# Optimization experiments

Measured on AMD Instinct MI355X. Metric: run time of the kernel, lower is better.

## Reference

```python
import jax, jax.numpy as jnp
import numpy as np

FS = 44100
RESAMPLING_FACTOR = 32
N_SINES = 256
TWO_PI = 2.0 * np.pi


def linear_upsample(x, scale):
    """Match torch F.interpolate(mode='linear', align_corners=False) with integer scale_factor.
    x: [B, C, N] -> [B, C, N*scale]
    """
    n = x.shape[-1]
    out_n = n * scale
    # source coordinate for each output index (area-pixel convention)
    src = (jnp.arange(out_n, dtype=jnp.float32) + 0.5) / scale - 0.5
    src = jnp.clip(src, 0.0, n - 1)
    i0 = jnp.floor(src).astype(jnp.int32)
    i1 = jnp.minimum(i0 + 1, n - 1)
    w = (src - i0.astype(jnp.float32)).astype(x.dtype)
    return x[..., i0] * (1.0 - w) + x[..., i1] * w


def setup_inputs() -> dict:
    key = jax.random.key(0)
    k1, k2 = jax.random.split(key)
    B, S, N = 4, N_SINES, 512
    # realistic audible frequencies and normalized amplitudes
    frequencies = jax.random.uniform(k1, (B, S, N), dtype=jnp.float32) * 5000.0 + 40.0
    amplitudes = jax.random.uniform(k2, (B, S, N), dtype=jnp.float32) / S
    return {"frequencies": frequencies, "amplitudes": amplitudes}


def reference(frequencies, amplitudes):
    # upsample control signals: [B, S, N] -> [B, S, N*R]
    freqs_up = linear_upsample(frequencies, RESAMPLING_FACTOR)
    amps_up = linear_upsample(amplitudes, RESAMPLING_FACTOR)
    omegas = freqs_up * (TWO_PI / FS)
    phases = jnp.cumsum(omegas, axis=-1)
    phases = phases % TWO_PI
    # weighted sum over sines, keepdim -> [B, 1, N*R]
    signal = jnp.sum(amps_up * jnp.sin(phases), axis=1, keepdims=True)
    return signal
```

## Files before the change

### kernel.cpp

```cpp
#include <hip/hip_runtime.h>
#include <hip/hip_bf16.h>

constexpr int S = 256;
constexpr int N = 512;
constexpr int R = 32;
constexpr int OUT_N = N * R;

__global__ __launch_bounds__(512) void block_prefix_kernel(
    const float* __restrict__ freq, double* __restrict__ G) {
  const int row = blockIdx.x;
  const int n = threadIdx.x;
  const float* f = freq + (size_t)row * N;

  __shared__ double sh[N];
  float fn  = f[n];
  float fnp = (n < N - 1) ? f[n + 1] : 0.0f;
  sh[n] = (n < N - 1) ? 16.0 * ((double)fn + (double)fnp) : 0.0;
  __syncthreads();

  for (int off = 1; off < N; off <<= 1) {
    double add = (n >= off) ? sh[n - off] : 0.0;
    __syncthreads();
    sh[n] += add;
    __syncthreads();
  }

  double g = 16.0 * (double)f[0] + ((n == 0) ? 0.0 : sh[n - 1]);
  G[(size_t)row * N + n] = g;
}

__global__ __launch_bounds__(256) void synth_kernel(
    const float* __restrict__ freq, const float* __restrict__ amp,
    const double* __restrict__ G, float* __restrict__ out) {
  const int tid = threadIdx.x;
  const int split = tid >> 6;
  const int samp = tid & 63;
  const int gid = blockIdx.x * 64 + samp;
  const int b = gid >> 14;
  const int j = gid & (OUT_N - 1);

  int n;
  double c1, c2, gsel;
  float wa;
  if (j < 16) {
    n = 0; c1 = (double)(j + 1); c2 = 0.0; gsel = 0.0; wa = 0.0f;
  } else if (j >= OUT_N - 16) {
    n = N - 1; c1 = (double)(j - (OUT_N - 16) + 1); c2 = 0.0; gsel = 1.0; wa = 0.0f;
  } else {
    const int jj = j - 16;
    n = jj >> 5;
    const int k = jj & 31;
    c1 = (double)(k + 1);
    c2 = (double)((k + 1) * (k + 1)) * (1.0 / 64.0);
    gsel = 1.0;
    wa = ((float)k + 0.5f) * (1.0f / 32.0f);
  }
  const int dn1 = min(n + 1, N - 1) - n;

  const float* frow = freq + ((size_t)b * S) * N + n;
  const float* arow = amp  + ((size_t)b * S) * N + n;
  const double* grow = G   + ((size_t)b * S) * N + n;

  const double inv_fs = 1.0 / 44100.0;
  float acc = 0.0f;
  const int s0 = split * (S / 4);
  #pragma unroll 4
  for (int s = s0; s < s0 + S / 4; ++s) {
    const float* fp = frow + (size_t)s * N;
    const float* ap = arow + (size_t)s * N;
    const float fn  = fp[0];
    const float fn1 = fp[dn1];
    const float an  = ap[0];
    const float an1 = ap[dn1];
    const double g = grow[(size_t)s * N];

    double ph = fma(gsel, g, fma(c1, (double)fn,
                                 c2 * ((double)fn1 - (double)fn)));
    double r = ph * inv_fs;
    r -= floor(r);
    const float sv = __builtin_amdgcn_sinf((float)r);
    const float av = fmaf(an1 - an, wa, an);
    acc = fmaf(av, sv, acc);
  }

  __shared__ float red[256];
  red[tid] = acc;
  __syncthreads();
  if (tid < 64) {
    const float v = red[tid] + red[tid + 64] + red[tid + 128] + red[tid + 192];
    out[gid] = v;
  }
}

extern "C" void kernel_launch(void* const* d_in, const int* in_sizes, int n_in,
                              void* d_out, int out_size, void* d_ws, size_t ws_size,
                              hipStream_t stream) {
  const float* freq = (const float*)d_in[0];
  const float* amp  = (const float*)d_in[1];
  float* out = (float*)d_out;
  double* G = (double*)d_ws;

  const int B = in_sizes[0] / (S * N);

  block_prefix_kernel<<<dim3(B * S), dim3(512), 0, stream>>>(freq, G);
  synth_kernel<<<dim3(B * OUT_N / 64), dim3(256), 0, stream>>>(freq, amp, G, out);
}
```

Baseline: 78.17 us.

## Pack per-segment phase and amplitude data, reduce phase mod in prep, use fp32 synth

The prefix kernel now uses one wavefront per row with a serial per-thread scan plus shuffle scan. It reduces the cumulative phase modulo the sample rate in double, then writes an interleaved 8-float record (phase, f, df, a, da) per control point. The synth kernel then reads one packed record per sine and evaluates the phase polynomial in fp32 instead of fp64. It also uses 512-thread blocks splitting sines across 8 waves. This removes fp64 arithmetic and scattered loads from the hot loop, at the cost of some fp32 phase precision and a larger workspace.

```diff
diff --git a/kernel.cpp b/kernel.cpp
--- a/kernel.cpp
+++ b/kernel.cpp
@@ -1,37 +1,67 @@
 #include <hip/hip_runtime.h>
-#include <hip/hip_bf16.h>
 
 constexpr int S = 256;
 constexpr int N = 512;
 constexpr int R = 32;
 constexpr int OUT_N = N * R;
 
-__global__ __launch_bounds__(512) void block_prefix_kernel(
-    const float* __restrict__ freq, double* __restrict__ G) {
+__global__ __launch_bounds__(64) void prep_pack_kernel(
+    const float* __restrict__ freq, const float* __restrict__ amp,
+    float* __restrict__ W) {
   const int row = blockIdx.x;
-  const int n = threadIdx.x;
-  const float* f = freq + (size_t)row * N;
+  const int l = threadIdx.x;
+  const float* f = freq + (size_t)row * N + l * 8;
+  const float* a = amp  + (size_t)row * N + l * 8;
 
-  __shared__ double sh[N];
-  float fn  = f[n];
-  float fnp = (n < N - 1) ? f[n + 1] : 0.0f;
-  sh[n] = (n < N - 1) ? 16.0 * ((double)fn + (double)fnp) : 0.0;
-  __syncthreads();
+  const float4 fa = *reinterpret_cast<const float4*>(f);
+  const float4 fb = *reinterpret_cast<const float4*>(f + 4);
+  const float4 aa = *reinterpret_cast<const float4*>(a);
+  const float4 ab = *reinterpret_cast<const float4*>(a + 4);
 
-  for (int off = 1; off < N; off <<= 1) {
-    double add = (n >= off) ? sh[n - off] : 0.0;
-    __syncthreads();
-    sh[n] += add;
-    __syncthreads();
+  float fv[9] = {fa.x, fa.y, fa.z, fa.w, fb.x, fb.y, fb.z, fb.w, 0.0f};
+  float av[9] = {aa.x, aa.y, aa.z, aa.w, ab.x, ab.y, ab.z, ab.w, 0.0f};
+  fv[8] = __shfl_down(fa.x, 1);
+  av[8] = __shfl_down(aa.x, 1);
+
+  double p[8];
+  double run = 0.0;
+  #pragma unroll
+  for (int i = 0; i < 8; ++i) {
+    const int n = l * 8 + i;
+    const double inc =
+        (n < N - 1) ? 16.0 * ((double)fv[i] + (double)fv[i + 1]) : 0.0;
+    run += inc;
+    p[i] = run;
   }
 
-  double g = 16.0 * (double)f[0] + ((n == 0) ? 0.0 : sh[n - 1]);
-  G[(size_t)row * N + n] = g;
+  double x = run;
+  #pragma unroll
+  for (int off = 1; off < 64; off <<= 1) {
+    const double y = __shfl_up(x, off);
+    if (l >= off) x += y;
+  }
+  const double excl = x - run;
+  const float f0 = __shfl(fa.x, 0);
+  const double base = 16.0 * (double)f0;
+
+  float* wrow = W + ((size_t)row * N + l * 8) * 8;
+  #pragma unroll
+  for (int i = 0; i < 8; ++i) {
+    const int n = l * 8 + i;
+    const double g = base + excl + (i ? p[i - 1] : 0.0);
+    const double gm = g - floor(g / 44100.0) * 44100.0;
+    const float fn = fv[i];
+    const float df = (n < N - 1) ? fv[i + 1] - fn : 0.0f;
+    const float an = av[i];
+    const float da = (n < N - 1) ? av[i + 1] - an : 0.0f;
+    const float4 o{(float)gm, fn, df, an};
+    *reinterpret_cast<float4*>(wrow + i * 8) = o;
+    wrow[i * 8 + 4] = da;
+  }
 }
 
-__global__ __launch_bounds__(256) void synth_kernel(
-    const float* __restrict__ freq, const float* __restrict__ amp,
-    const double* __restrict__ G, float* __restrict__ out) {
+__global__ __launch_bounds__(512) void synth_sin_kernel(
+    const float* __restrict__ W, float* __restrict__ out) {
   const int tid = threadIdx.x;
   const int split = tid >> 6;
   const int samp = tid & 63;
@@ -40,54 +70,43 @@
   const int j = gid & (OUT_N - 1);
 
   int n;
-  double c1, c2, gsel;
-  float wa;
+  float c1, c2, wa;
   if (j < 16) {
-    n = 0; c1 = (double)(j + 1); c2 = 0.0; gsel = 0.0; wa = 0.0f;
+    n = 0; c1 = (float)(j - 15); c2 = 0.0f; wa = 0.0f;
   } else if (j >= OUT_N - 16) {
-    n = N - 1; c1 = (double)(j - (OUT_N - 16) + 1); c2 = 0.0; gsel = 1.0; wa = 0.0f;
+    n = N - 1; c1 = (float)(j - (OUT_N - 16) + 1); c2 = 0.0f; wa = 0.0f;
   } else {
     const int jj = j - 16;
     n = jj >> 5;
     const int k = jj & 31;
-    c1 = (double)(k + 1);
-    c2 = (double)((k + 1) * (k + 1)) * (1.0 / 64.0);
-    gsel = 1.0;
+    c1 = (float)(k + 1);
+    c2 = (float)((k + 1) * (k + 1)) * (1.0f / 64.0f);
     wa = ((float)k + 0.5f) * (1.0f / 32.0f);
   }
-  const int dn1 = min(n + 1, N - 1) - n;
 
-  const float* frow = freq + ((size_t)b * S) * N + n;
-  const float* arow = amp  + ((size_t)b * S) * N + n;
-  const double* grow = G   + ((size_t)b * S) * N + n;
-
-  const double inv_fs = 1.0 / 44100.0;
+  const float* wp = W + (((size_t)b * S + split * (S / 8)) * N + n) * 8;
+  constexpr float inv_fs = 1.0f / 44100.0f;
   float acc = 0.0f;
-  const int s0 = split * (S / 4);
-  #pragma unroll 4
-  for (int s = s0; s < s0 + S / 4; ++s) {
-    const float* fp = frow + (size_t)s * N;
-    const float* ap = arow + (size_t)s * N;
-    const float fn  = fp[0];
-    const float fn1 = fp[dn1];
-    const float an  = ap[0];
-    const float an1 = ap[dn1];
-    const double g = grow[(size_t)s * N];
-
-    double ph = fma(gsel, g, fma(c1, (double)fn,
-                                 c2 * ((double)fn1 - (double)fn)));
-    double r = ph * inv_fs;
-    r -= floor(r);
-    const float sv = __builtin_amdgcn_sinf((float)r);
-    const float av = fmaf(an1 - an, wa, an);
+  #pragma unroll 8
+  for (int s = 0; s < S / 8; ++s) {
+    const float4 v = *reinterpret_cast<const float4*>(wp);
+    const float da = wp[4];
+    float P = fmaf(c2, v.z, fmaf(c1, v.y, v.x));
+    float r = P * inv_fs;
+    r = r - floorf(r);
+    const float sv = __builtin_amdgcn_sinf(r);
+    const float av = fmaf(da, wa, v.w);
     acc = fmaf(av, sv, acc);
+    wp += (size_t)N * 8;
   }
 
-  __shared__ float red[256];
+  __shared__ float red[512];
   red[tid] = acc;
   __syncthreads();
   if (tid < 64) {
-    const float v = red[tid] + red[tid + 64] + red[tid + 128] + red[tid + 192];
+    float v = 0.0f;
+    #pragma unroll
+    for (int c = 0; c < 8; ++c) v += red[tid + 64 * c];
     out[gid] = v;
   }
 }
@@ -98,10 +117,10 @@
   const float* freq = (const float*)d_in[0];
   const float* amp  = (const float*)d_in[1];
   float* out = (float*)d_out;
-  double* G = (double*)d_ws;
+  float* W = (float*)d_ws;
 
   const int B = in_sizes[0] / (S * N);
 
-  block_prefix_kernel<<<dim3(B * S), dim3(512), 0, stream>>>(freq, G);
-  synth_kernel<<<dim3(B * OUT_N / 64), dim3(256), 0, stream>>>(freq, amp, G, out);
+  prep_pack_kernel<<<dim3(B * S), dim3(64), 0, stream>>>(freq, amp, W);
+  synth_sin_kernel<<<dim3(B * OUT_N / 64), dim3(512), 0, stream>>>(W, out);
 }
```

After: 79.87 us. +2.2%, slower.
